# Kernel optimization log

Measured on AMD Instinct MI355X. Metric: run time of the kernel, lower is better.

Reference implementation:

```python
import jax, jax.numpy as jnp
import numpy as np

D = 512          # embedding_dim (cfg.hidden_size)
K = 1024         # codebook_size
DECAY = 0.99
EPS = 1e-05
COMMITMENT_COST = 0.25


def setup_inputs() -> dict:
    key = jax.random.key(0)
    k1, k2, k3 = jax.random.split(key, 3)
    return {
        "inputs": jax.random.normal(k1, (32, 1024, D), dtype=jnp.float32),
        "embedding_weight": jax.random.normal(k2, (K, D), dtype=jnp.float32),
        "ema_cluster_size": jnp.zeros((K,), dtype=jnp.float32),
        "ema_w": jax.random.normal(k3, (K, D), dtype=jnp.float32),
    }


def reference(inputs, embedding_weight, ema_cluster_size, ema_w):
    input_shape = inputs.shape
    flat = inputs.reshape(-1, D)  # [N, D]

    # Squared L2 distances to every codebook entry: [N, K]
    distances = (
        jnp.sum(flat ** 2, axis=1, keepdims=True)
        + jnp.sum(embedding_weight ** 2, axis=1)
        - 2.0 * flat @ embedding_weight.T
    )
    idx = jnp.argmin(distances, axis=1)                      # [N]
    encodings = jax.nn.one_hot(idx, K, dtype=flat.dtype)     # [N, K]

    # ---- EMA codebook update (training path) ----
    counts = jnp.sum(encodings, axis=0)                      # == bincount(idx)
    new_cs = ema_cluster_size * DECAY + (1.0 - DECAY) * counts
    n = jnp.sum(new_cs)
    new_cs = (new_cs + EPS) / (n + K * EPS) * n              # Laplace smoothing
    # dw = encodings.T @ flat, done as a fused gather-reduce instead of dense matmul
    dw = jax.ops.segment_sum(flat, idx, num_segments=K)      # [K, D]
    new_ema_w = ema_w * DECAY + (1.0 - DECAY) * dw
    new_embedding = new_ema_w / new_cs[:, None]              # updated codebook

    # quantized = encodings @ new_embedding, expressed as a gather
    quantized = new_embedding[idx].reshape(input_shape)

    e_latent_loss = jnp.mean((jax.lax.stop_gradient(quantized) - inputs) ** 2)
    loss = COMMITMENT_COST * e_latent_loss

    # straight-through estimator
    quantized = inputs + jax.lax.stop_gradient(quantized - inputs)

    avg_probs = jnp.mean(encodings, axis=0)
    perplexity = jnp.exp(-jnp.sum(avg_probs * jnp.log(avg_probs + 1e-10)))
    return (loss, quantized, perplexity, encodings)
```

## Files before the change

### kernel.cpp

```cpp
#include <hip/hip_runtime.h>

#define NROWS 32768
#define DIM   512
#define KC    1024

typedef __attribute__((ext_vector_type(8)))  short short8v;
typedef __attribute__((ext_vector_type(16))) float f32x16;

__global__ __launch_bounds__(256) void k_enorm(const float* __restrict__ E,
                                               float* __restrict__ en2) {
    int w = threadIdx.x >> 6, lane = threadIdx.x & 63;
    int c = blockIdx.x * 4 + w;
    const float* row = E + (size_t)c * DIM;
    float4 a = *reinterpret_cast<const float4*>(&row[lane * 8]);
    float4 b = *reinterpret_cast<const float4*>(&row[lane * 8 + 4]);
    float s = a.x*a.x + a.y*a.y + a.z*a.z + a.w*a.w
            + b.x*b.x + b.y*b.y + b.z*b.z + b.w*b.w;
    #pragma unroll
    for (int off = 32; off; off >>= 1) s += __shfl_xor(s, off);
    if (!lane) en2[c] = s;
}

__device__ __forceinline__ void split_bf16(float v, short& hi, short& lo) {
    unsigned u = __float_as_uint(v);
    unsigned r = u + 0x7FFFu + ((u >> 16) & 1u);
    hi = (short)(r >> 16);
    float hif = __uint_as_float(r & 0xFFFF0000u);
    float rem = v - hif;
    unsigned u2 = __float_as_uint(rem);
    unsigned r2 = u2 + 0x7FFFu + ((u2 >> 16) & 1u);
    lo = (short)(r2 >> 16);
}

__device__ __forceinline__ unsigned long long pack_key(float d, int c) {
    unsigned u = __float_as_uint(d);
    u = (u & 0x80000000u) ? ~u : (u | 0x80000000u);
    return ((unsigned long long)u << 32) | (unsigned)c;
}

__global__ __launch_bounds__(256) void k_split(const float* __restrict__ x,
                                               const float* __restrict__ E,
                                               short* __restrict__ xfrag,
                                               short* __restrict__ efrag) {
    __shared__ short hbuf[32][520];
    __shared__ short lbuf[32][520];
    int b = blockIdx.x, t = threadIdx.x;
    const float* src;
    short* dst;
    if (b < NROWS / 32) {
        src = x + (size_t)b * 32 * DIM;
        dst = xfrag + (size_t)b * 32768;
    } else {
        src = E + (size_t)(b - NROWS / 32) * 32 * DIM;
        dst = efrag + (size_t)(b - NROWS / 32) * 32768;
    }
    #pragma unroll
    for (int f = 0; f < 16; ++f) {
        int u = t + f * 256;
        int row = u >> 7, c4 = (u & 127) * 4;
        float4 v = *reinterpret_cast<const float4*>(&src[row * DIM + c4]);
        short4 h4, l4;
        split_bf16(v.x, h4.x, l4.x); split_bf16(v.y, h4.y, l4.y);
        split_bf16(v.z, h4.z, l4.z); split_bf16(v.w, h4.w, l4.w);
        *reinterpret_cast<short4*>(&hbuf[row][c4]) = h4;
        *reinterpret_cast<short4*>(&lbuf[row][c4]) = l4;
    }
    __syncthreads();
    #pragma unroll
    for (int f = 0; f < 16; ++f) {
        int u = t + f * 256;
        int lane = u & 63, h = (u >> 6) & 1, kb = u >> 7;
        int row = lane & 31, k0 = kb * 16 + (lane >> 5) * 8;
        const short* s = h ? &lbuf[row][k0] : &hbuf[row][k0];
        short8v val = *reinterpret_cast<const short8v*>(s);
        *reinterpret_cast<short8v*>(&dst[(size_t)u * 8]) = val;
    }
}

__global__ __launch_bounds__(256, 2) void k_argmin(const short* __restrict__ xfrag,
                                                   const short* __restrict__ efrag,
                                                   const float* __restrict__ en2,
                                                   unsigned long long* __restrict__ packed) {
    __shared__ short sbuf[2][24 * 512];
    const int tid = threadIdx.x;
    const int w = tid >> 6, l = tid & 63;
    const int wr = w >> 1, wc = w & 1;
    const int l31 = l & 31, lh = l >> 5;

    int bid = blockIdx.x;
    int xcd = bid & 7, j = bid >> 3;
    int row0 = (xcd * 32 + (j >> 2)) * 128;
    int c0   = (j & 3) * 256;

    const short* srcbase[6];
    #pragma unroll
    for (int s = 0; s < 6; ++s) {
        int q = s * 4 + (tid >> 6);
        int g = q >> 1, h = q & 1;
        const short* base = (g < 4)
            ? xfrag + (size_t)(row0 / 32 + g) * 32768
            : efrag + (size_t)(c0 / 32 + (g - 4)) * 32768;
        srcbase[s] = base + h * 512 + (tid & 63) * 8;
    }
    const int stq = tid >> 6;
    const int stl = (tid & 63) * 8;

    f32x16 acc[2][4];
    #pragma unroll
    for (int a = 0; a < 2; ++a)
        #pragma unroll
        for (int b = 0; b < 4; ++b)
            #pragma unroll
            for (int r = 0; r < 16; ++r) acc[a][b][r] = 0.f;

    {
        short8v st[6];
        #pragma unroll
        for (int s = 0; s < 6; ++s)
            st[s] = *reinterpret_cast<const short8v*>(srcbase[s]);
        #pragma unroll
        for (int s = 0; s < 6; ++s)
            *reinterpret_cast<short8v*>(&sbuf[0][(s * 4 + stq) * 512 + stl]) = st[s];
    }
    __syncthreads();

    for (int kb = 0; kb < 32; ++kb) {
        const int cur = kb & 1;
        short8v st[6];
        if (kb < 31) {
            #pragma unroll
            for (int s = 0; s < 6; ++s)
                st[s] = *reinterpret_cast<const short8v*>(
                    srcbase[s] + (size_t)(kb + 1) * 1024);
        }
        short8v ah[2], al[2], bh[4], bl[4];
        const short* sb = sbuf[cur];
        #pragma unroll
        for (int m = 0; m < 2; ++m) {
            int g = wr * 2 + m;
            ah[m] = *reinterpret_cast<const short8v*>(&sb[(g * 2 + 0) * 512 + l * 8]);
            al[m] = *reinterpret_cast<const short8v*>(&sb[(g * 2 + 1) * 512 + l * 8]);
        }
        #pragma unroll
        for (int n = 0; n < 4; ++n) {
            int g = 4 + wc * 4 + n;
            bh[n] = *reinterpret_cast<const short8v*>(&sb[(g * 2 + 0) * 512 + l * 8]);
            bl[n] = *reinterpret_cast<const short8v*>(&sb[(g * 2 + 1) * 512 + l * 8]);
        }
        #pragma unroll
        for (int m = 0; m < 2; ++m)
            #pragma unroll
            for (int n = 0; n < 4; ++n) {
                acc[m][n] = __builtin_amdgcn_mfma_f32_32x32x16_bf16(
                    ah[m], bh[n], acc[m][n], 0, 0, 0);
                acc[m][n] = __builtin_amdgcn_mfma_f32_32x32x16_bf16(
                    ah[m], bl[n], acc[m][n], 0, 0, 0);
                acc[m][n] = __builtin_amdgcn_mfma_f32_32x32x16_bf16(
                    al[m], bh[n], acc[m][n], 0, 0, 0);
            }
        if (kb < 31) {
            #pragma unroll
            for (int s = 0; s < 6; ++s)
                *reinterpret_cast<short8v*>(
                    &sbuf[cur ^ 1][(s * 4 + stq) * 512 + stl]) = st[s];
        }
        __syncthreads();
    }

    float e2[4];
    #pragma unroll
    for (int n = 0; n < 4; ++n) e2[n] = en2[c0 + wc * 128 + n * 32 + l31];
    #pragma unroll
    for (int m = 0; m < 2; ++m) {
        #pragma unroll
        for (int r = 0; r < 16; ++r) {
            unsigned long long key = 0xFFFFFFFFFFFFFFFFull;
            #pragma unroll
            for (int n = 0; n < 4; ++n) {
                float d = fmaf(-2.f, acc[m][n][r], e2[n]);
                unsigned long long k = pack_key(d, c0 + wc * 128 + n * 32 + l31);
                if (k < key) key = k;
            }
            #pragma unroll
            for (int off = 1; off < 32; off <<= 1) {
                unsigned long long o = __shfl_xor(key, off);
                if (o < key) key = o;
            }
            if (l31 == 0) {
                int grow = row0 + wr * 64 + m * 32 + (r & 3) + 8 * (r >> 2) + 4 * lh;
                atomicMin(&packed[grow], key);
            }
        }
    }
}

__global__ __launch_bounds__(256) void k_hist(const unsigned long long* __restrict__ packed,
                                              int* __restrict__ idx,
                                              int* __restrict__ counts) {
    __shared__ int h[KC];
    for (int i = threadIdx.x; i < KC; i += 256) h[i] = 0;
    __syncthreads();
    int g = blockIdx.x * 256 + threadIdx.x;
    int c = (int)(unsigned)(packed[g] & 0xFFFFFFFFull);
    idx[g] = c;
    atomicAdd(&h[c], 1);
    __syncthreads();
    for (int i = threadIdx.x; i < KC; i += 256)
        if (h[i]) atomicAdd(&counts[i], h[i]);
}

__global__ __launch_bounds__(1024) void k_meta(const int* __restrict__ counts,
                                               const float* __restrict__ ema_cs,
                                               float* __restrict__ smoothed,
                                               int* __restrict__ offsets,
                                               int* __restrict__ cursor,
                                               float* __restrict__ perp_out) {
    __shared__ float red[KC];
    __shared__ int sc[KC];
    int t = threadIdx.x;
    int cnt = counts[t];
    float cs = ema_cs[t] * 0.99f + 0.01f * (float)cnt;
    red[t] = cs; __syncthreads();
    for (int s = 512; s; s >>= 1) { if (t < s) red[t] += red[t + s]; __syncthreads(); }
    float n = red[0];
    __syncthreads();
    float sm = (cs + 1e-5f) / (n + 1024.f * 1e-5f) * n;
    smoothed[t] = sm;
    float p = (float)cnt / 32768.f;
    red[t] = p * logf(p + 1e-10f);
    __syncthreads();
    for (int s = 512; s; s >>= 1) { if (t < s) red[t] += red[t + s]; __syncthreads(); }
    if (!t) perp_out[0] = expf(-red[0]);
    sc[t] = cnt; __syncthreads();
    for (int s = 1; s < KC; s <<= 1) {
        int v = (t >= s) ? sc[t - s] : 0;
        __syncthreads();
        sc[t] += v;
        __syncthreads();
    }
    int off = sc[t] - cnt;
    offsets[t] = off;
    cursor[t] = off;
}

__global__ __launch_bounds__(256) void k_scatter(const int* __restrict__ idx,
                                                 int* __restrict__ cursor,
                                                 int* __restrict__ bucket) {
    int g = blockIdx.x * 256 + threadIdx.x;
    int c = idx[g];
    int pos = atomicAdd(&cursor[c], 1);
    bucket[pos] = g;
}

__global__ __launch_bounds__(256) void k_dw(const float* __restrict__ x,
                                            const float* __restrict__ ema_w,
                                            const int* __restrict__ offsets,
                                            const int* __restrict__ counts,
                                            const int* __restrict__ bucket,
                                            const float* __restrict__ smoothed,
                                            float* __restrict__ newE) {
    __shared__ int rows[256];
    int k = blockIdx.x, t = threadIdx.x;
    int beg = offsets[k], m = counts[k];
    float a0 = 0.f, a1 = 0.f;
    for (int base = 0; base < m; base += 256) {
        int n = min(256, m - base);
        __syncthreads();
        if (t < n) rows[t] = bucket[beg + base + t];
        __syncthreads();
        int i = 0;
        for (; i + 4 <= n; i += 4) {
            int r0 = rows[i], r1 = rows[i + 1], r2 = rows[i + 2], r3 = rows[i + 3];
            float v00 = x[(size_t)r0 * DIM + t];
            float v01 = x[(size_t)r0 * DIM + t + 256];
            float v10 = x[(size_t)r1 * DIM + t];
            float v11 = x[(size_t)r1 * DIM + t + 256];
            float v20 = x[(size_t)r2 * DIM + t];
            float v21 = x[(size_t)r2 * DIM + t + 256];
            float v30 = x[(size_t)r3 * DIM + t];
            float v31 = x[(size_t)r3 * DIM + t + 256];
            a0 += v00 + v10 + v20 + v30;
            a1 += v01 + v11 + v21 + v31;
        }
        for (; i < n; ++i) {
            int r = rows[i];
            a0 += x[(size_t)r * DIM + t];
            a1 += x[(size_t)r * DIM + t + 256];
        }
    }
    float sm = smoothed[k];
    newE[(size_t)k * DIM + t]       = (ema_w[(size_t)k * DIM + t]       * 0.99f + 0.01f * a0) / sm;
    newE[(size_t)k * DIM + t + 256] = (ema_w[(size_t)k * DIM + t + 256] * 0.99f + 0.01f * a1) / sm;
}

__global__ __launch_bounds__(256) void k_qe(const float* __restrict__ x,
                                            const int* __restrict__ idx,
                                            const float* __restrict__ newE,
                                            float* __restrict__ outq,
                                            float* __restrict__ enc,
                                            float* __restrict__ partials) {
    int b = blockIdx.x, t = threadIdx.x;
    int row8 = b * 8;
    float lp = 0.f;
    #pragma unroll
    for (int it = 0; it < 4; ++it) {
        int slot = t + it * 256;
        int r = slot >> 7;
        int c4 = (slot & 127) * 4;
        int row = row8 + r;
        int code = idx[row];
        float4 in = *reinterpret_cast<const float4*>(&x[(size_t)row * DIM + c4]);
        float4 q  = *reinterpret_cast<const float4*>(&newE[(size_t)code * DIM + c4]);
        float4 d;
        d.x = q.x - in.x; d.y = q.y - in.y; d.z = q.z - in.z; d.w = q.w - in.w;
        float4 o;
        o.x = in.x + d.x; o.y = in.y + d.y; o.z = in.z + d.z; o.w = in.w + d.w;
        *reinterpret_cast<float4*>(&outq[(size_t)row * DIM + c4]) = o;
        lp += d.x*d.x + d.y*d.y + d.z*d.z + d.w*d.w;
    }
    {
        int er = row8 + (t >> 5);
        int l32 = t & 31;
        int one = idx[er];
        float4* dst = reinterpret_cast<float4*>(enc + (size_t)er * KC);
        #pragma unroll
        for (int s = 0; s < 8; ++s) {
            int c4 = l32 + s * 32;
            int base = c4 * 4;
            float4 v;
            v.x = (one == base)     ? 1.f : 0.f;
            v.y = (one == base + 1) ? 1.f : 0.f;
            v.z = (one == base + 2) ? 1.f : 0.f;
            v.w = (one == base + 3) ? 1.f : 0.f;
            dst[c4] = v;
        }
    }
    #pragma unroll
    for (int off = 32; off; off >>= 1) lp += __shfl_xor(lp, off);
    __shared__ float wr[4];
    int lane = t & 63, w = t >> 6;
    if (!lane) wr[w] = lp;
    __syncthreads();
    if (t == 0) partials[b] = wr[0] + wr[1] + wr[2] + wr[3];
}

__global__ __launch_bounds__(256) void k_lossfin(const float* __restrict__ partials,
                                                 float* __restrict__ out0) {
    __shared__ double red[256];
    double s = 0.0;
    for (int i = threadIdx.x; i < 4096; i += 256) s += (double)partials[i];
    red[threadIdx.x] = s; __syncthreads();
    for (int st = 128; st; st >>= 1) {
        if (threadIdx.x < st) red[threadIdx.x] += red[threadIdx.x + st];
        __syncthreads();
    }
    if (!threadIdx.x) out0[0] = (float)(0.25 * red[0] / 16777216.0);
}

extern "C" void kernel_launch(void* const* d_in, const int* in_sizes, int n_in,
                              void* d_out, int out_size, void* d_ws, size_t ws_size,
                              hipStream_t stream) {
    const float* x   = (const float*)d_in[0];
    const float* E   = (const float*)d_in[1];
    const float* ecs = (const float*)d_in[2];
    const float* emw = (const float*)d_in[3];
    float* out = (float*)d_out;

    char* ws = (char*)d_ws;
    int*   idx      = (int*)(ws + 0);
    int*   bucket   = (int*)(ws + 131072);
    float* en2      = (float*)(ws + 262144);
    int*   counts   = (int*)(ws + 266240);
    int*   offsets  = (int*)(ws + 270336);
    int*   cursor   = (int*)(ws + 274432);
    float* smoothed = (float*)(ws + 278528);
    float* newE     = (float*)(ws + 282624);
    float* partials = (float*)(ws + 282624 + 2097152);
    unsigned long long* packed = (unsigned long long*)newE;

    float* out_loss = out;
    float* out_q    = out + 1;
    float* out_perp = out + 16777217;
    float* out_enc  = out + 16777218;

    short* xfrag = (short*)out_enc;
    short* efrag = xfrag + (size_t)NROWS * DIM * 2;

    hipMemsetAsync(counts, 0, KC * sizeof(int), stream);
    hipMemsetAsync(packed, 0xFF, NROWS * sizeof(unsigned long long), stream);

    k_enorm  <<<KC / 4, 256, 0, stream>>>(E, en2);
    k_split  <<<NROWS / 32 + KC / 32, 256, 0, stream>>>(x, E, xfrag, efrag);
    k_argmin <<<(NROWS / 128) * 4, 256, 0, stream>>>(xfrag, efrag, en2, packed);
    k_hist   <<<NROWS / 256, 256, 0, stream>>>(packed, idx, counts);
    k_meta   <<<1, 1024, 0, stream>>>(counts, ecs, smoothed, offsets, cursor, out_perp);
    k_scatter<<<NROWS / 256, 256, 0, stream>>>(idx, cursor, bucket);
    k_dw     <<<KC, 256, 0, stream>>>(x, emw, offsets, counts, bucket, smoothed, newE);
    k_qe     <<<NROWS / 8, 256, 0, stream>>>(x, idx, newE, out_q, out_enc, partials);
    k_lossfin<<<1, 256, 0, stream>>>(partials, out_loss);
}
```

Before: 314.7 us.

## Use direct global-to-LDS loads with triple-buffered pipeline in argmin GEMM

Replaces the register-staged global loads and LDS stores in the distance GEMM main loop with global_load_lds direct-to-LDS transfers. The double buffer becomes a three-stage ring that prefetches two K-blocks ahead, with explicit vmcnt waits and raw barriers. The aim is to free staging registers and VALU/LDS-store work and to hide more global latency behind the MFMAs. In exchange, LDS use per block rises by half, and correctness now depends on the hand-written waitcnt and barrier placement.

```diff
diff --git a/kernel.cpp b/kernel.cpp
--- a/kernel.cpp
+++ b/kernel.cpp
@@ -6,6 +6,9 @@
 
 typedef __attribute__((ext_vector_type(8)))  short short8v;
 typedef __attribute__((ext_vector_type(16))) float f32x16;
+
+#define AS1 __attribute__((address_space(1)))
+#define AS3 __attribute__((address_space(3)))
 
 __global__ __launch_bounds__(256) void k_enorm(const float* __restrict__ E,
                                                float* __restrict__ en2) {
@@ -81,7 +84,7 @@
                                                    const short* __restrict__ efrag,
                                                    const float* __restrict__ en2,
                                                    unsigned long long* __restrict__ packed) {
-    __shared__ short sbuf[2][24 * 512];
+    __shared__ short sbuf[3][12288];
     const int tid = threadIdx.x;
     const int w = tid >> 6, l = tid & 63;
     const int wr = w >> 1, wc = w & 1;
@@ -92,18 +95,15 @@
     int row0 = (xcd * 32 + (j >> 2)) * 128;
     int c0   = (j & 3) * 256;
 
-    const short* srcbase[6];
+    const short* gsrc[6];
     #pragma unroll
     for (int s = 0; s < 6; ++s) {
-        int q = s * 4 + (tid >> 6);
-        int g = q >> 1, h = q & 1;
+        int q = s * 4 + w, g = q >> 1, h = q & 1;
         const short* base = (g < 4)
             ? xfrag + (size_t)(row0 / 32 + g) * 32768
             : efrag + (size_t)(c0 / 32 + (g - 4)) * 32768;
-        srcbase[s] = base + h * 512 + (tid & 63) * 8;
-    }
-    const int stq = tid >> 6;
-    const int stl = (tid & 63) * 8;
+        gsrc[s] = base + h * 512 + l * 8;
+    }
 
     f32x16 acc[2][4];
     #pragma unroll
@@ -113,26 +113,63 @@
             #pragma unroll
             for (int r = 0; r < 16; ++r) acc[a][b][r] = 0.f;
 
-    {
-        short8v st[6];
+    #pragma unroll
+    for (int s = 0; s < 6; ++s)
+        __builtin_amdgcn_global_load_lds((const AS1 void*)gsrc[s],
+                                         (AS3 void*)&sbuf[0][(s * 4 + w) * 512],
+                                         16, 0, 0);
+    #pragma unroll
+    for (int s = 0; s < 6; ++s)
+        __builtin_amdgcn_global_load_lds((const AS1 void*)(gsrc[s] + 1024),
+                                         (AS3 void*)&sbuf[1][(s * 4 + w) * 512],
+                                         16, 0, 0);
+    asm volatile("s_waitcnt vmcnt(6)" ::: "memory");
+    __builtin_amdgcn_s_barrier();
+    __builtin_amdgcn_sched_barrier(0);
+
+    #pragma unroll 3
+    for (int kb = 0; kb < 30; ++kb) {
+        const int cur = kb % 3, nxt = (kb + 2) % 3;
         #pragma unroll
         for (int s = 0; s < 6; ++s)
-            st[s] = *reinterpret_cast<const short8v*>(srcbase[s]);
-        #pragma unroll
-        for (int s = 0; s < 6; ++s)
-            *reinterpret_cast<short8v*>(&sbuf[0][(s * 4 + stq) * 512 + stl]) = st[s];
-    }
-    __syncthreads();
-
-    for (int kb = 0; kb < 32; ++kb) {
-        const int cur = kb & 1;
-        short8v st[6];
-        if (kb < 31) {
-            #pragma unroll
-            for (int s = 0; s < 6; ++s)
-                st[s] = *reinterpret_cast<const short8v*>(
-                    srcbase[s] + (size_t)(kb + 1) * 1024);
-        }
+            __builtin_amdgcn_global_load_lds(
+                (const AS1 void*)(gsrc[s] + (size_t)(kb + 2) * 1024),
+                (AS3 void*)&sbuf[nxt][(s * 4 + w) * 512], 16, 0, 0);
+        {
+            short8v ah[2], al[2], bh[4], bl[4];
+            const short* sb = sbuf[cur];
+            #pragma unroll
+            for (int m = 0; m < 2; ++m) {
+                int g = wr * 2 + m;
+                ah[m] = *reinterpret_cast<const short8v*>(&sb[(g * 2 + 0) * 512 + l * 8]);
+                al[m] = *reinterpret_cast<const short8v*>(&sb[(g * 2 + 1) * 512 + l * 8]);
+            }
+            #pragma unroll
+            for (int n = 0; n < 4; ++n) {
+                int g = 4 + wc * 4 + n;
+                bh[n] = *reinterpret_cast<const short8v*>(&sb[(g * 2 + 0) * 512 + l * 8]);
+                bl[n] = *reinterpret_cast<const short8v*>(&sb[(g * 2 + 1) * 512 + l * 8]);
+            }
+            #pragma unroll
+            for (int m = 0; m < 2; ++m)
+                #pragma unroll
+                for (int n = 0; n < 4; ++n) {
+                    acc[m][n] = __builtin_amdgcn_mfma_f32_32x32x16_bf16(
+                        ah[m], bh[n], acc[m][n], 0, 0, 0);
+                    acc[m][n] = __builtin_amdgcn_mfma_f32_32x32x16_bf16(
+                        ah[m], bl[n], acc[m][n], 0, 0, 0);
+                    acc[m][n] = __builtin_amdgcn_mfma_f32_32x32x16_bf16(
+                        al[m], bh[n], acc[m][n], 0, 0, 0);
+                }
+        }
+        asm volatile("s_waitcnt vmcnt(6) lgkmcnt(0)" ::: "memory");
+        __builtin_amdgcn_s_barrier();
+        __builtin_amdgcn_sched_barrier(0);
+    }
+
+    #pragma unroll
+    for (int e = 0; e < 2; ++e) {
+        const int kb = 30 + e, cur = kb % 3;
         short8v ah[2], al[2], bh[4], bl[4];
         const short* sb = sbuf[cur];
         #pragma unroll
@@ -158,13 +195,11 @@
                 acc[m][n] = __builtin_amdgcn_mfma_f32_32x32x16_bf16(
                     al[m], bh[n], acc[m][n], 0, 0, 0);
             }
-        if (kb < 31) {
-            #pragma unroll
-            for (int s = 0; s < 6; ++s)
-                *reinterpret_cast<short8v*>(
-                    &sbuf[cur ^ 1][(s * 4 + stq) * 512 + stl]) = st[s];
-        }
-        __syncthreads();
+        if (e == 0) {
+            asm volatile("s_waitcnt vmcnt(0) lgkmcnt(0)" ::: "memory");
+            __builtin_amdgcn_s_barrier();
+            __builtin_amdgcn_sched_barrier(0);
+        }
     }
 
     float e2[4];
```

Result: no change. 310.0 us (-1.5%).
